# Optimization experiments

Hardware: AMD Instinct MI355X
Metric: run time of the kernel (lower is better)

The kernel has to match this reference:

```python
import jax, jax.numpy as jnp
import numpy as np

E, H, FF = 1024, 16, 4096
HD = E // H
B, S = 4, 2048


def _ln(x, g, b, eps=1e-5):
    m = jnp.mean(x, axis=-1, keepdims=True)
    v = jnp.mean((x - m) ** 2, axis=-1, keepdims=True)
    return (x - m) / jnp.sqrt(v + eps) * g + b


def setup_inputs() -> dict:
    k = jax.random.key(0)
    ks = jax.random.split(k, 12)
    sd = 0.02
    return {
        "value": jax.random.normal(ks[0], (B, S, E), jnp.float32),
        "key": jax.random.normal(ks[1], (B, S, E), jnp.float32),
        "query": jax.random.normal(ks[2], (B, S, E), jnp.float32),
        "mask": jnp.ones((B, 1, 1, S), jnp.int32),
        "Wv": sd * jax.random.normal(ks[3], (E, E), jnp.float32),
        "Wk": sd * jax.random.normal(ks[4], (E, E), jnp.float32),
        "Wq": sd * jax.random.normal(ks[5], (E, E), jnp.float32),
        "Wo": sd * jax.random.normal(ks[6], (E, E), jnp.float32),
        "bo": jnp.zeros((E,), jnp.float32),
        "ln1_g": jnp.ones((E,), jnp.float32), "ln1_b": jnp.zeros((E,), jnp.float32),
        "ln2_g": jnp.ones((E,), jnp.float32), "ln2_b": jnp.zeros((E,), jnp.float32),
        "lnf_g": jnp.ones((E,), jnp.float32), "lnf_b": jnp.zeros((E,), jnp.float32),
        "W1": sd * jax.random.normal(ks[7], (E, FF), jnp.float32),
        "b1": jnp.zeros((FF,), jnp.float32),
        "W2": sd * jax.random.normal(ks[8], (FF, E), jnp.float32),
        "b2": jnp.zeros((E,), jnp.float32),
    }


def reference(value, key, query, mask, Wv, Wk, Wq, Wo, bo,
              ln1_g, ln1_b, ln2_g, ln2_b, lnf_g, lnf_b, W1, b1, W2, b2):
    N, Sq, Em = query.shape
    # pre-norms (value & key share prenorm2 params, as in the torch module)
    v = _ln(value, ln2_g, ln2_b)
    k = _ln(key, ln2_g, ln2_b)
    q = _ln(query, ln1_g, ln1_b)
    # QKV projections (no bias), split heads
    V = (v @ Wv).reshape(N, v.shape[1], H, HD)
    K = (k @ Wk).reshape(N, k.shape[1], H, HD)
    Q = (q @ Wq).reshape(N, Sq, H, HD)
    energy = jnp.einsum("nqhd,nkhd->nhqk", Q, K)  # [N,H,Sq,Sk]
    energy = jnp.where(mask == 0, jnp.float32(-1e20), energy)
    attn = jax.nn.softmax(energy / jnp.float32(HD ** 0.5), axis=-1)
    out = jnp.einsum("nhqk,nkhd->nqhd", attn, V).reshape(N, Sq, Em)
    out = out @ Wo + bo
    x = out + q  # residual (drop_path is identity in eval)
    f = _ln(x, lnf_g, lnf_b) @ W1 + b1
    f = jax.nn.gelu(f, approximate=False) @ W2 + b2
    return f + x
```

## Files before the change

### kernel.cpp

```cpp
#include <hip/hip_runtime.h>
#include <hip/hip_bf16.h>
#include <math.h>

typedef __bf16 bf16x8 __attribute__((ext_vector_type(8)));
typedef __bf16 bf16x4 __attribute__((ext_vector_type(4)));
typedef float f32x4 __attribute__((ext_vector_type(4)));

#define AS1 __attribute__((address_space(1)))
#define AS3 __attribute__((address_space(3)))

__device__ __forceinline__ void gll16(const __bf16* g, __bf16* l) {
    __builtin_amdgcn_global_load_lds((const AS1 unsigned int*)g,
                                     (AS3 unsigned int*)l, 16, 0, 0);
}

__global__ __launch_bounds__(256) void transpose_w(const float* __restrict__ W,
                                                   __bf16* __restrict__ Wt,
                                                   int K, int N) {
    __shared__ float tile[32][33];
    int n0 = blockIdx.x * 32, k0 = blockIdx.y * 32;
    int tx = threadIdx.x & 31, ty = threadIdx.x >> 5;
    #pragma unroll
    for (int j = ty; j < 32; j += 8)
        tile[j][tx] = W[(size_t)(k0 + j) * N + n0 + tx];
    __syncthreads();
    #pragma unroll
    for (int j = ty; j < 32; j += 8)
        Wt[(size_t)(n0 + j) * K + k0 + tx] = (__bf16)tile[tx][j];
}

__global__ __launch_bounds__(256) void ln_kernel(const float* __restrict__ x,
                                                 const float* __restrict__ g,
                                                 const float* __restrict__ bb,
                                                 float* __restrict__ out32,
                                                 __bf16* __restrict__ outbf) {
    const int E = 1024;
    size_t row = blockIdx.x;
    int t = threadIdx.x;
    const float4* xr = (const float4*)(x + row * E);
    float4 v = xr[t];
    float s  = v.x + v.y + v.z + v.w;
    float s2 = v.x * v.x + v.y * v.y + v.z * v.z + v.w * v.w;
    #pragma unroll
    for (int off = 32; off >= 1; off >>= 1) {
        s  += __shfl_down(s, off);
        s2 += __shfl_down(s2, off);
    }
    __shared__ float red[2][4];
    int wid = t >> 6, lane = t & 63;
    if (lane == 0) { red[0][wid] = s; red[1][wid] = s2; }
    __syncthreads();
    if (t == 0) {
        float S1 = red[0][0] + red[0][1] + red[0][2] + red[0][3];
        float S2 = red[1][0] + red[1][1] + red[1][2] + red[1][3];
        float mean = S1 / E;
        float var  = S2 / E - mean * mean;
        red[0][0] = mean;
        red[1][0] = 1.0f / sqrtf(var + 1e-5f);
    }
    __syncthreads();
    float mean = red[0][0], rstd = red[1][0];
    float4 gv = ((const float4*)g)[t];
    float4 bv = ((const float4*)bb)[t];
    float y0 = (v.x - mean) * rstd * gv.x + bv.x;
    float y1 = (v.y - mean) * rstd * gv.y + bv.y;
    float y2 = (v.z - mean) * rstd * gv.z + bv.z;
    float y3 = (v.w - mean) * rstd * gv.w + bv.w;
    if (out32) ((float4*)(out32 + row * E))[t] = make_float4(y0, y1, y2, y3);
    if (outbf) {
        bf16x4 o;
        o[0] = (__bf16)y0; o[1] = (__bf16)y1; o[2] = (__bf16)y2; o[3] = (__bf16)y3;
        ((bf16x4*)(outbf + row * E))[t] = o;
    }
}

template <int EPI>
__global__ __launch_bounds__(256) void gemm128(const __bf16* __restrict__ A,
                                               const __bf16* __restrict__ Bt,
                                               const float* __restrict__ bias,
                                               const float* __restrict__ resid,
                                               void* __restrict__ Cout,
                                               int M, int N, int K) {
    __shared__ __bf16 As[128 * 64];
    __shared__ __bf16 Bs[128 * 64];
    int tid  = threadIdx.x;
    int lane = tid & 63, wid = tid >> 6;
    int quad = lane >> 4, l15 = lane & 15;
    int waveM = wid >> 1, waveN = wid & 1;
    size_t rowBase = (size_t)blockIdx.y * 128;
    size_t colBase = (size_t)blockIdx.x * 128;

    int lrow8  = lane >> 3;
    int lchunk = (lane & 7) ^ lrow8;
    const __bf16* Ag0 = A  + (rowBase + wid * 32 + lrow8) * (size_t)K + lchunk * 8;
    const __bf16* Bg0 = Bt + (colBase + wid * 32 + lrow8) * (size_t)K + lchunk * 8;
    __bf16* AsB = &As[(wid * 32) * 64];
    __bf16* BsB = &Bs[(wid * 32) * 64];

    f32x4 acc[4][4] = {};
    int swz = l15 & 7;

    for (int kb = 0; kb < K; kb += 64) {
        __syncthreads();
        #pragma unroll
        for (int i = 0; i < 4; i++) {
            gll16(Ag0 + (size_t)i * 8 * K + kb, AsB + i * 512);
            gll16(Bg0 + (size_t)i * 8 * K + kb, BsB + i * 512);
        }
        __syncthreads();
        #pragma unroll
        for (int ks = 0; ks < 2; ks++) {
            int p = ((ks * 4 + quad) ^ swz) * 8;
            bf16x8 af[4], bfr[4];
            #pragma unroll
            for (int mi = 0; mi < 4; mi++) {
                int m = waveM * 64 + mi * 16 + l15;
                af[mi] = *(const bf16x8*)&As[m * 64 + p];
            }
            #pragma unroll
            for (int ni = 0; ni < 4; ni++) {
                int n = waveN * 64 + ni * 16 + l15;
                bfr[ni] = *(const bf16x8*)&Bs[n * 64 + p];
            }
            #pragma unroll
            for (int mi = 0; mi < 4; mi++)
                #pragma unroll
                for (int ni = 0; ni < 4; ni++)
                    acc[mi][ni] = __builtin_amdgcn_mfma_f32_16x16x32_bf16(
                        af[mi], bfr[ni], acc[mi][ni], 0, 0, 0);
        }
    }

    #pragma unroll
    for (int mi = 0; mi < 4; mi++)
    #pragma unroll
    for (int ni = 0; ni < 4; ni++) {
        size_t col = colBase + waveN * 64 + ni * 16 + l15;
        if (EPI == 3) {
            size_t m0 = rowBase + waveM * 64 + mi * 16 + quad * 4;
            bf16x4 pk;
            #pragma unroll
            for (int r = 0; r < 4; r++) pk[r] = (__bf16)acc[mi][ni][r];
            *(bf16x4*)((__bf16*)Cout + col * M + m0) = pk;
        } else {
            #pragma unroll
            for (int r = 0; r < 4; r++) {
                size_t row = rowBase + waveM * 64 + mi * 16 + quad * 4 + r;
                float v = acc[mi][ni][r];
                if (EPI == 1) {
                    ((float*)Cout)[row * N + col] = v + bias[col] + resid[row * N + col];
                } else if (EPI == 2) {
                    float t2 = v + bias[col];
                    float gl = 0.5f * t2 * (1.0f + erff(t2 * 0.70710678118654752f));
                    ((__bf16*)Cout)[row * N + col] = (__bf16)gl;
                } else {
                    ((__bf16*)Cout)[row * N + col] = (__bf16)v;
                }
            }
        }
    }
}

__global__ __launch_bounds__(256) void attn_kernel(const __bf16* __restrict__ Q,
                                                   const __bf16* __restrict__ Kg,
                                                   const __bf16* __restrict__ Vt,
                                                   const int* __restrict__ mask,
                                                   __bf16* __restrict__ Out) {
    const int S = 2048, E = 1024, M = 8192;
    int qt = blockIdx.x, bh = blockIdx.y;
    int b = bh >> 4, h = bh & 15;
    int q0 = qt * 128;
    int tid = threadIdx.x, lane = tid & 63, wid = tid >> 6;
    int quad = lane >> 4, l15 = lane & 15;

    __shared__ __bf16 Ks[64][72];
    __shared__ __bf16 Vs[64][72];
    __shared__ __bf16 Ps[128][68];

    bf16x8 aq[2][2];
    #pragma unroll
    for (int m = 0; m < 2; m++)
        #pragma unroll
        for (int ks = 0; ks < 2; ks++) {
            size_t row = (size_t)(b * S + q0 + wid * 32 + m * 16 + l15);
            aq[m][ks] = *(const bf16x8*)(Q + row * E + h * 64 + ks * 32 + quad * 8);
        }

    int srow = tid >> 2;
    int scol = (tid & 3) * 16;
    const __bf16* Kbase = Kg + (size_t)(b * S) * E + h * 64;
    const __bf16* Vbase = Vt + (size_t)(h * 64 + srow) * M + b * S;

    bf16x8 kp0, kp1, vp0, vp1;
    kp0 = *(const bf16x8*)(Kbase + (size_t)srow * E + scol);
    kp1 = *(const bf16x8*)(Kbase + (size_t)srow * E + scol + 8);
    vp0 = *(const bf16x8*)(Vbase + scol);
    vp1 = *(const bf16x8*)(Vbase + scol + 8);

    f32x4 accO[2][4] = {};
    float accl[2][4] = {};

    for (int kt = 0; kt < S / 64; kt++) {
        int k0 = kt * 64;
        __syncthreads();
        *(bf16x8*)&Ks[srow][scol]     = kp0;
        *(bf16x8*)&Ks[srow][scol + 8] = kp1;
        *(bf16x8*)&Vs[srow][scol]     = vp0;
        *(bf16x8*)&Vs[srow][scol + 8] = vp1;
        __syncthreads();
        if (kt + 1 < S / 64) {
            int kn = k0 + 64;
            kp0 = *(const bf16x8*)(Kbase + (size_t)(kn + srow) * E + scol);
            kp1 = *(const bf16x8*)(Kbase + (size_t)(kn + srow) * E + scol + 8);
            vp0 = *(const bf16x8*)(Vbase + kn + scol);
            vp1 = *(const bf16x8*)(Vbase + kn + scol + 8);
        }

        f32x4 sa[2][4];
        #pragma unroll
        for (int nt = 0; nt < 4; nt++) {
            bf16x8 b0 = *(const bf16x8*)&Ks[nt * 16 + l15][quad * 8];
            bf16x8 b1 = *(const bf16x8*)&Ks[nt * 16 + l15][32 + quad * 8];
            #pragma unroll
            for (int m = 0; m < 2; m++) {
                f32x4 a = {};
                a = __builtin_amdgcn_mfma_f32_16x16x32_bf16(aq[m][0], b0, a, 0, 0, 0);
                a = __builtin_amdgcn_mfma_f32_16x16x32_bf16(aq[m][1], b1, a, 0, 0, 0);
                sa[m][nt] = a;
            }
        }

        #pragma unroll
        for (int nt = 0; nt < 4; nt++) {
            bool mz = (mask[b * S + k0 + nt * 16 + l15] == 0);
            #pragma unroll
            for (int m = 0; m < 2; m++)
                #pragma unroll
                for (int r = 0; r < 4; r++) {
                    float p = mz ? 0.0f : __expf(sa[m][nt][r] * 0.125f);
                    accl[m][r] += p;
                    Ps[wid * 32 + m * 16 + quad * 4 + r][nt * 16 + l15] = (__bf16)p;
                }
        }

        bf16x8 ap[2][2];
        #pragma unroll
        for (int m = 0; m < 2; m++)
            #pragma unroll
            for (int ks = 0; ks < 2; ks++)
                ap[m][ks] = *(const bf16x8*)&Ps[wid * 32 + m * 16 + l15][ks * 32 + quad * 8];

        #pragma unroll
        for (int nt = 0; nt < 4; nt++) {
            bf16x8 bv0 = *(const bf16x8*)&Vs[nt * 16 + l15][quad * 8];
            bf16x8 bv1 = *(const bf16x8*)&Vs[nt * 16 + l15][32 + quad * 8];
            #pragma unroll
            for (int m = 0; m < 2; m++) {
                accO[m][nt] = __builtin_amdgcn_mfma_f32_16x16x32_bf16(ap[m][0], bv0, accO[m][nt], 0, 0, 0);
                accO[m][nt] = __builtin_amdgcn_mfma_f32_16x16x32_bf16(ap[m][1], bv1, accO[m][nt], 0, 0, 0);
            }
        }
    }

    #pragma unroll
    for (int m = 0; m < 2; m++)
        #pragma unroll
        for (int r = 0; r < 4; r++) {
            float l = accl[m][r];
            #pragma unroll
            for (int off = 1; off < 16; off <<= 1) l += __shfl_xor(l, off);
            accl[m][r] = 1.0f / l;
        }

    #pragma unroll
    for (int m = 0; m < 2; m++)
        #pragma unroll
        for (int nt = 0; nt < 4; nt++)
            #pragma unroll
            for (int r = 0; r < 4; r++) {
                size_t row = (size_t)(b * S + q0 + wid * 32 + m * 16 + quad * 4 + r);
                Out[row * E + h * 64 + nt * 16 + l15] =
                    (__bf16)(accO[m][nt][r] * accl[m][r]);
            }
}

extern "C" void kernel_launch(void* const* d_in, const int* in_sizes, int n_in,
                              void* d_out, int out_size, void* d_ws, size_t ws_size,
                              hipStream_t stream) {
    const int Bb = 4, S = 2048, E = 1024, FF = 4096;
    const int M = Bb * S;

    const float* value = (const float*)d_in[0];
    const float* key   = (const float*)d_in[1];
    const float* query = (const float*)d_in[2];
    const int*   mask  = (const int*)d_in[3];
    const float* Wv    = (const float*)d_in[4];
    const float* Wk    = (const float*)d_in[5];
    const float* Wq    = (const float*)d_in[6];
    const float* Wo    = (const float*)d_in[7];
    const float* bo    = (const float*)d_in[8];
    const float* ln1_g = (const float*)d_in[9];
    const float* ln1_b = (const float*)d_in[10];
    const float* ln2_g = (const float*)d_in[11];
    const float* ln2_b = (const float*)d_in[12];
    const float* lnf_g = (const float*)d_in[13];
    const float* lnf_b = (const float*)d_in[14];
    const float* W1    = (const float*)d_in[15];
    const float* b1    = (const float*)d_in[16];
    const float* W2    = (const float*)d_in[17];
    const float* b2    = (const float*)d_in[18];

    char* ws = (char*)d_ws;
    const size_t MB = 1024 * 1024;
    __bf16* Wqt = (__bf16*)(ws + 0 * MB);
    __bf16* Wkt = (__bf16*)(ws + 2 * MB);
    __bf16* Wvt = (__bf16*)(ws + 4 * MB);
    __bf16* Wot = (__bf16*)(ws + 6 * MB);
    __bf16* W1t = (__bf16*)(ws + 8 * MB);
    __bf16* W2t = (__bf16*)(ws + 16 * MB);
    __bf16* q_bf = (__bf16*)(ws + 24 * MB);
    __bf16* k_bf = (__bf16*)(ws + 40 * MB);
    __bf16* v_bf = (__bf16*)(ws + 56 * MB);
    __bf16* Qb   = (__bf16*)(ws + 72 * MB);
    __bf16* Kb   = (__bf16*)(ws + 88 * MB);
    __bf16* Vtg  = (__bf16*)(ws + 104 * MB);
    __bf16* attn = q_bf;
    __bf16* x_ln = k_bf;
    __bf16* h1   = v_bf;
    float*  qln  = (float*)(ws + 120 * MB);
    float*  x32  = (float*)(ws + 152 * MB);

    transpose_w<<<dim3(E / 32, E / 32), 256, 0, stream>>>(Wq, Wqt, E, E);
    transpose_w<<<dim3(E / 32, E / 32), 256, 0, stream>>>(Wk, Wkt, E, E);
    transpose_w<<<dim3(E / 32, E / 32), 256, 0, stream>>>(Wv, Wvt, E, E);
    transpose_w<<<dim3(E / 32, E / 32), 256, 0, stream>>>(Wo, Wot, E, E);
    transpose_w<<<dim3(FF / 32, E / 32), 256, 0, stream>>>(W1, W1t, E, FF);
    transpose_w<<<dim3(E / 32, FF / 32), 256, 0, stream>>>(W2, W2t, FF, E);

    ln_kernel<<<M, 256, 0, stream>>>(query, ln1_g, ln1_b, qln, q_bf);
    ln_kernel<<<M, 256, 0, stream>>>(key, ln2_g, ln2_b, nullptr, k_bf);
    ln_kernel<<<M, 256, 0, stream>>>(value, ln2_g, ln2_b, nullptr, v_bf);

    gemm128<0><<<dim3(E / 128, M / 128), 256, 0, stream>>>(q_bf, Wqt, nullptr, nullptr, Qb, M, E, E);
    gemm128<0><<<dim3(E / 128, M / 128), 256, 0, stream>>>(k_bf, Wkt, nullptr, nullptr, Kb, M, E, E);
    gemm128<3><<<dim3(E / 128, M / 128), 256, 0, stream>>>(v_bf, Wvt, nullptr, nullptr, Vtg, M, E, E);

    attn_kernel<<<dim3(S / 128, Bb * 16), 256, 0, stream>>>(Qb, Kb, Vtg, mask, attn);

    gemm128<1><<<dim3(E / 128, M / 128), 256, 0, stream>>>(attn, Wot, bo, qln, x32, M, E, E);

    ln_kernel<<<M, 256, 0, stream>>>(x32, lnf_g, lnf_b, nullptr, x_ln);

    gemm128<2><<<dim3(FF / 128, M / 128), 256, 0, stream>>>(x_ln, W1t, b1, nullptr, h1, M, FF, E);
    gemm128<1><<<dim3(E / 128, M / 128), 256, 0, stream>>>(h1, W2t, b2, x32, (float*)d_out, M, E, FF);
}
```

Measured before the change: 719.8 us.

## Merge launches, fuse Q/K GEMMs, and rework attention with register-resident P

```diff
diff --git a/kernel.cpp b/kernel.cpp
--- a/kernel.cpp
+++ b/kernel.cpp
@@ -14,11 +14,35 @@
                                      (AS3 unsigned int*)l, 16, 0, 0);
 }
 
-__global__ __launch_bounds__(256) void transpose_w(const float* __restrict__ W,
-                                                   __bf16* __restrict__ Wt,
-                                                   int K, int N) {
+__device__ __forceinline__ unsigned pkbf(float a, float b) {
+    union { __bf16 h[2]; unsigned u; } t;
+    t.h[0] = (__bf16)a; t.h[1] = (__bf16)b;
+    return t.u;
+}
+
+__global__ __launch_bounds__(256) void transpose_all(
+    const float* __restrict__ Wq, const float* __restrict__ Wk,
+    const float* __restrict__ Wv, const float* __restrict__ Wo,
+    const float* __restrict__ W1, const float* __restrict__ W2,
+    __bf16* __restrict__ Wqt, __bf16* __restrict__ Wkt,
+    __bf16* __restrict__ Wvt, __bf16* __restrict__ Wot,
+    __bf16* __restrict__ W1t, __bf16* __restrict__ W2t) {
+    int g = blockIdx.x;
+    const float* W; __bf16* Wt; int K, N, kt, nt;
+    if (g < 4096) {
+        int mi = g >> 10, loc = g & 1023;
+        K = 1024; N = 1024; kt = loc >> 5; nt = loc & 31;
+        W  = mi == 0 ? Wq  : mi == 1 ? Wk  : mi == 2 ? Wv  : Wo;
+        Wt = mi == 0 ? Wqt : mi == 1 ? Wkt : mi == 2 ? Wvt : Wot;
+    } else if (g < 8192) {
+        int loc = g - 4096; W = W1; Wt = W1t;
+        K = 1024; N = 4096; kt = loc >> 7; nt = loc & 127;
+    } else {
+        int loc = g - 8192; W = W2; Wt = W2t;
+        K = 4096; N = 1024; kt = loc >> 5; nt = loc & 31;
+    }
+    int k0 = kt * 32, n0 = nt * 32;
     __shared__ float tile[32][33];
-    int n0 = blockIdx.x * 32, k0 = blockIdx.y * 32;
     int tx = threadIdx.x & 31, ty = threadIdx.x >> 5;
     #pragma unroll
     for (int j = ty; j < 32; j += 8)
@@ -29,18 +53,26 @@
         Wt[(size_t)(n0 + j) * K + k0 + tx] = (__bf16)tile[tx][j];
 }
 
-__global__ __launch_bounds__(256) void ln_kernel(const float* __restrict__ x,
-                                                 const float* __restrict__ g,
-                                                 const float* __restrict__ bb,
-                                                 float* __restrict__ out32,
-                                                 __bf16* __restrict__ outbf) {
+__global__ __launch_bounds__(256) void ln3_kernel(
+    const float* __restrict__ q, const float* __restrict__ k,
+    const float* __restrict__ v,
+    const float* __restrict__ g1, const float* __restrict__ b1,
+    const float* __restrict__ g2, const float* __restrict__ b2,
+    float* __restrict__ qln, __bf16* __restrict__ qbf,
+    __bf16* __restrict__ kbf, __bf16* __restrict__ vbf) {
     const int E = 1024;
+    int which = blockIdx.y;
+    const float* x = which == 0 ? q : which == 1 ? k : v;
+    const float* g = which == 0 ? g1 : g2;
+    const float* bb = which == 0 ? b1 : b2;
+    float* o32 = which == 0 ? qln : nullptr;
+    __bf16* obf = which == 0 ? qbf : which == 1 ? kbf : vbf;
+
     size_t row = blockIdx.x;
     int t = threadIdx.x;
-    const float4* xr = (const float4*)(x + row * E);
-    float4 v = xr[t];
-    float s  = v.x + v.y + v.z + v.w;
-    float s2 = v.x * v.x + v.y * v.y + v.z * v.z + v.w * v.w;
+    float4 val = ((const float4*)(x + row * E))[t];
+    float s  = val.x + val.y + val.z + val.w;
+    float s2 = val.x * val.x + val.y * val.y + val.z * val.z + val.w * val.w;
     #pragma unroll
     for (int off = 32; off >= 1; off >>= 1) {
         s  += __shfl_down(s, off);
@@ -62,25 +94,65 @@
     float mean = red[0][0], rstd = red[1][0];
     float4 gv = ((const float4*)g)[t];
     float4 bv = ((const float4*)bb)[t];
-    float y0 = (v.x - mean) * rstd * gv.x + bv.x;
-    float y1 = (v.y - mean) * rstd * gv.y + bv.y;
-    float y2 = (v.z - mean) * rstd * gv.z + bv.z;
-    float y3 = (v.w - mean) * rstd * gv.w + bv.w;
-    if (out32) ((float4*)(out32 + row * E))[t] = make_float4(y0, y1, y2, y3);
-    if (outbf) {
-        bf16x4 o;
-        o[0] = (__bf16)y0; o[1] = (__bf16)y1; o[2] = (__bf16)y2; o[3] = (__bf16)y3;
-        ((bf16x4*)(outbf + row * E))[t] = o;
-    }
+    float y0 = (val.x - mean) * rstd * gv.x + bv.x;
+    float y1 = (val.y - mean) * rstd * gv.y + bv.y;
+    float y2 = (val.z - mean) * rstd * gv.z + bv.z;
+    float y3 = (val.w - mean) * rstd * gv.w + bv.w;
+    if (o32) ((float4*)(o32 + row * E))[t] = make_float4(y0, y1, y2, y3);
+    bf16x4 o;
+    o[0] = (__bf16)y0; o[1] = (__bf16)y1; o[2] = (__bf16)y2; o[3] = (__bf16)y3;
+    ((bf16x4*)(obf + row * E))[t] = o;
+}
+
+__global__ __launch_bounds__(256) void ln_kernel(const float* __restrict__ x,
+                                                 const float* __restrict__ g,
+                                                 const float* __restrict__ bb,
+                                                 __bf16* __restrict__ outbf) {
+    const int E = 1024;
+    size_t row = blockIdx.x;
+    int t = threadIdx.x;
+    float4 v = ((const float4*)(x + row * E))[t];
+    float s  = v.x + v.y + v.z + v.w;
+    float s2 = v.x * v.x + v.y * v.y + v.z * v.z + v.w * v.w;
+    #pragma unroll
+    for (int off = 32; off >= 1; off >>= 1) {
+        s  += __shfl_down(s, off);
+        s2 += __shfl_down(s2, off);
+    }
+    __shared__ float red[2][4];
+    int wid = t >> 6, lane = t & 63;
+    if (lane == 0) { red[0][wid] = s; red[1][wid] = s2; }
+    __syncthreads();
+    if (t == 0) {
+        float S1 = red[0][0] + red[0][1] + red[0][2] + red[0][3];
+        float S2 = red[1][0] + red[1][1] + red[1][2] + red[1][3];
+        float mean = S1 / E;
+        float var  = S2 / E - mean * mean;
+        red[0][0] = mean;
+        red[1][0] = 1.0f / sqrtf(var + 1e-5f);
+    }
+    __syncthreads();
+    float mean = red[0][0], rstd = red[1][0];
+    float4 gv = ((const float4*)g)[t];
+    float4 bv = ((const float4*)bb)[t];
+    bf16x4 o;
+    o[0] = (__bf16)((v.x - mean) * rstd * gv.x + bv.x);
+    o[1] = (__bf16)((v.y - mean) * rstd * gv.y + bv.y);
+    o[2] = (__bf16)((v.z - mean) * rstd * gv.z + bv.z);
+    o[3] = (__bf16)((v.w - mean) * rstd * gv.w + bv.w);
+    ((bf16x4*)(outbf + row * E))[t] = o;
 }
 
 template <int EPI>
 __global__ __launch_bounds__(256) void gemm128(const __bf16* __restrict__ A,
+                                               const __bf16* __restrict__ A2,
                                                const __bf16* __restrict__ Bt,
+                                               const __bf16* __restrict__ Bt2,
                                                const float* __restrict__ bias,
                                                const float* __restrict__ resid,
                                                void* __restrict__ Cout,
-                                               int M, int N, int K) {
+                                               int M, int N, int K,
+                                               int splitN, float scale) {
     __shared__ __bf16 As[128 * 64];
     __shared__ __bf16 Bs[128 * 64];
     int tid  = threadIdx.x;
@@ -90,6 +162,93 @@
     size_t rowBase = (size_t)blockIdx.y * 128;
     size_t colBase = (size_t)blockIdx.x * 128;
 
+    const __bf16* Ap = A; const __bf16* Bp = Bt;
+    size_t colLoc = colBase;
+    float sc = scale;
+    if ((int)colBase >= splitN) { Ap = A2; Bp = Bt2; colLoc = colBase - splitN; sc = 1.0f; }
+
+    int lrow8  = lane >> 3;
+    int lchunk = (lane & 7) ^ lrow8;
+    const __bf16* Ag0 = Ap + (rowBase + wid * 32 + lrow8) * (size_t)K + lchunk * 8;
+    const __bf16* Bg0 = Bp + (colLoc  + wid * 32 + lrow8) * (size_t)K + lchunk * 8;
+    __bf16* AsB = &As[(wid * 32) * 64];
+    __bf16* BsB = &Bs[(wid * 32) * 64];
+
+    f32x4 acc[4][4] = {};
+    int swz = l15 & 7;
+
+    for (int kb = 0; kb < K; kb += 64) {
+        __syncthreads();
+        #pragma unroll
+        for (int i = 0; i < 4; i++) {
+            gll16(Ag0 + (size_t)i * 8 * K + kb, AsB + i * 512);
+            gll16(Bg0 + (size_t)i * 8 * K + kb, BsB + i * 512);
+        }
+        __syncthreads();
+        #pragma unroll
+        for (int ks = 0; ks < 2; ks++) {
+            int p = ((ks * 4 + quad) ^ swz) * 8;
+            bf16x8 af[4], bfr[4];
+            #pragma unroll
+            for (int mi = 0; mi < 4; mi++)
+                af[mi] = *(const bf16x8*)&As[(waveM * 64 + mi * 16 + l15) * 64 + p];
+            #pragma unroll
+            for (int ni = 0; ni < 4; ni++)
+                bfr[ni] = *(const bf16x8*)&Bs[(waveN * 64 + ni * 16 + l15) * 64 + p];
+            #pragma unroll
+            for (int mi = 0; mi < 4; mi++)
+                #pragma unroll
+                for (int ni = 0; ni < 4; ni++)
+                    acc[mi][ni] = __builtin_amdgcn_mfma_f32_16x16x32_bf16(
+                        bfr[ni], af[mi], acc[mi][ni], 0, 0, 0);
+        }
+    }
+
+    #pragma unroll
+    for (int mi = 0; mi < 4; mi++)
+    #pragma unroll
+    for (int ni = 0; ni < 4; ni++) {
+        size_t row = rowBase + waveM * 64 + mi * 16 + l15;
+        size_t col = colBase + waveN * 64 + ni * 16 + quad * 4;
+        f32x4 v = acc[mi][ni];
+        if (EPI == 1) {
+            float4 b4 = *(const float4*)&bias[col];
+            float4 r4 = *(const float4*)&resid[row * N + col];
+            float4 o;
+            o.x = v[0] + b4.x + r4.x; o.y = v[1] + b4.y + r4.y;
+            o.z = v[2] + b4.z + r4.z; o.w = v[3] + b4.w + r4.w;
+            *(float4*)&((float*)Cout)[row * N + col] = o;
+        } else if (EPI == 2) {
+            float4 b4 = *(const float4*)&bias[col];
+            bf16x4 pk;
+            #pragma unroll
+            for (int r = 0; r < 4; r++) {
+                float t2 = v[r] + ((const float*)&b4)[r];
+                pk[r] = (__bf16)(0.5f * t2 * (1.0f + erff(t2 * 0.70710678118654752f)));
+            }
+            *(bf16x4*)&((__bf16*)Cout)[row * N + col] = pk;
+        } else {
+            bf16x4 pk;
+            #pragma unroll
+            for (int r = 0; r < 4; r++) pk[r] = (__bf16)(v[r] * sc);
+            *(bf16x4*)&((__bf16*)Cout)[row * N + col] = pk;
+        }
+    }
+}
+
+__global__ __launch_bounds__(256) void gemmV(const __bf16* __restrict__ A,
+                                             const __bf16* __restrict__ Bt,
+                                             __bf16* __restrict__ Cout,
+                                             int M, int N, int K) {
+    __shared__ __bf16 As[128 * 64];
+    __shared__ __bf16 Bs[128 * 64];
+    int tid  = threadIdx.x;
+    int lane = tid & 63, wid = tid >> 6;
+    int quad = lane >> 4, l15 = lane & 15;
+    int waveM = wid >> 1, waveN = wid & 1;
+    size_t rowBase = (size_t)blockIdx.y * 128;
+    size_t colBase = (size_t)blockIdx.x * 128;
+
     int lrow8  = lane >> 3;
     int lchunk = (lane & 7) ^ lrow8;
     const __bf16* Ag0 = A  + (rowBase + wid * 32 + lrow8) * (size_t)K + lchunk * 8;
@@ -113,15 +272,11 @@
             int p = ((ks * 4 + quad) ^ swz) * 8;
             bf16x8 af[4], bfr[4];
             #pragma unroll
-            for (int mi = 0; mi < 4; mi++) {
-                int m = waveM * 64 + mi * 16 + l15;
-                af[mi] = *(const bf16x8*)&As[m * 64 + p];
-            }
-            #pragma unroll
-            for (int ni = 0; ni < 4; ni++) {
-                int n = waveN * 64 + ni * 16 + l15;
-                bfr[ni] = *(const bf16x8*)&Bs[n * 64 + p];
-            }
+            for (int mi = 0; mi < 4; mi++)
+                af[mi] = *(const bf16x8*)&As[(waveM * 64 + mi * 16 + l15) * 64 + p];
+            #pragma unroll
+            for (int ni = 0; ni < 4; ni++)
+                bfr[ni] = *(const bf16x8*)&Bs[(waveN * 64 + ni * 16 + l15) * 64 + p];
             #pragma unroll
             for (int mi = 0; mi < 4; mi++)
                 #pragma unroll
@@ -136,152 +291,160 @@
     #pragma unroll
     for (int ni = 0; ni < 4; ni++) {
         size_t col = colBase + waveN * 64 + ni * 16 + l15;
-        if (EPI == 3) {
-            size_t m0 = rowBase + waveM * 64 + mi * 16 + quad * 4;
-            bf16x4 pk;
-            #pragma unroll
-            for (int r = 0; r < 4; r++) pk[r] = (__bf16)acc[mi][ni][r];
-            *(bf16x4*)((__bf16*)Cout + col * M + m0) = pk;
-        } else {
-            #pragma unroll
-            for (int r = 0; r < 4; r++) {
-                size_t row = rowBase + waveM * 64 + mi * 16 + quad * 4 + r;
-                float v = acc[mi][ni][r];
-                if (EPI == 1) {
-                    ((float*)Cout)[row * N + col] = v + bias[col] + resid[row * N + col];
-                } else if (EPI == 2) {
-                    float t2 = v + bias[col];
-                    float gl = 0.5f * t2 * (1.0f + erff(t2 * 0.70710678118654752f));
-                    ((__bf16*)Cout)[row * N + col] = (__bf16)gl;
-                } else {
-                    ((__bf16*)Cout)[row * N + col] = (__bf16)v;
-                }
-            }
-        }
-    }
-}
-
-__global__ __launch_bounds__(256) void attn_kernel(const __bf16* __restrict__ Q,
-                                                   const __bf16* __restrict__ Kg,
+        size_t m0  = rowBase + waveM * 64 + mi * 16 + quad * 4;
+        bf16x4 pk;
+        #pragma unroll
+        for (int r = 0; r < 4; r++) pk[r] = (__bf16)acc[mi][ni][r];
+        *(bf16x4*)&Cout[col * M + m0] = pk;
+    }
+}
+
+__global__ __launch_bounds__(256) void attn_kernel(const __bf16* __restrict__ QK,
                                                    const __bf16* __restrict__ Vt,
                                                    const int* __restrict__ mask,
                                                    __bf16* __restrict__ Out) {
-    const int S = 2048, E = 1024, M = 8192;
+    const int S = 2048, E = 1024, E2 = 2048, M = 8192;
     int qt = blockIdx.x, bh = blockIdx.y;
     int b = bh >> 4, h = bh & 15;
     int q0 = qt * 128;
     int tid = threadIdx.x, lane = tid & 63, wid = tid >> 6;
     int quad = lane >> 4, l15 = lane & 15;
 
-    __shared__ __bf16 Ks[64][72];
-    __shared__ __bf16 Vs[64][72];
-    __shared__ __bf16 Ps[128][68];
+    __shared__ __bf16 KV[2][2 * 4096];
 
     bf16x8 aq[2][2];
     #pragma unroll
     for (int m = 0; m < 2; m++)
         #pragma unroll
-        for (int ks = 0; ks < 2; ks++) {
+        for (int hh = 0; hh < 2; hh++) {
             size_t row = (size_t)(b * S + q0 + wid * 32 + m * 16 + l15);
-            aq[m][ks] = *(const bf16x8*)(Q + row * E + h * 64 + ks * 32 + quad * 8);
-        }
-
-    int srow = tid >> 2;
-    int scol = (tid & 3) * 16;
-    const __bf16* Kbase = Kg + (size_t)(b * S) * E + h * 64;
-    const __bf16* Vbase = Vt + (size_t)(h * 64 + srow) * M + b * S;
-
-    bf16x8 kp0, kp1, vp0, vp1;
-    kp0 = *(const bf16x8*)(Kbase + (size_t)srow * E + scol);
-    kp1 = *(const bf16x8*)(Kbase + (size_t)srow * E + scol + 8);
-    vp0 = *(const bf16x8*)(Vbase + scol);
-    vp1 = *(const bf16x8*)(Vbase + scol + 8);
+            aq[m][hh] = *(const bf16x8*)(QK + row * E2 + h * 64 + hh * 32 + quad * 8);
+        }
+
+    int lrow8  = lane >> 3;
+    int lchunk = (lane & 7) ^ lrow8;
+    const __bf16* Kg0 = QK + (size_t)(b * S + wid * 16 + lrow8) * E2 + 1024 + h * 64 + lchunk * 8;
+    const __bf16* Vg0 = Vt + (size_t)(h * 64 + wid * 16 + lrow8) * M + b * S + lchunk * 8;
+
+    int srcA = ((quad & 1) * 2) * 16 + l15;
+    int srcB = srcA + 16;
+    bool selHi = (quad >= 2);
+    int swz = l15 & 7;
 
     f32x4 accO[2][4] = {};
-    float accl[2][4] = {};
+    float accl[2] = {0.f, 0.f};
+
+    {
+        __bf16* Kd = &KV[0][(wid * 16) * 64];
+        __bf16* Vd = &KV[0][4096 + (wid * 16) * 64];
+        #pragma unroll
+        for (int i = 0; i < 2; i++) {
+            gll16(Kg0 + (size_t)i * 8 * E2, Kd + i * 512);
+            gll16(Vg0 + (size_t)i * 8 * M,  Vd + i * 512);
+        }
+    }
+    __syncthreads();
 
     for (int kt = 0; kt < S / 64; kt++) {
         int k0 = kt * 64;
-        __syncthreads();
-        *(bf16x8*)&Ks[srow][scol]     = kp0;
-        *(bf16x8*)&Ks[srow][scol + 8] = kp1;
-        *(bf16x8*)&Vs[srow][scol]     = vp0;
-        *(bf16x8*)&Vs[srow][scol + 8] = vp1;
-        __syncthreads();
+        int buf = kt & 1;
         if (kt + 1 < S / 64) {
             int kn = k0 + 64;
-            kp0 = *(const bf16x8*)(Kbase + (size_t)(kn + srow) * E + scol);
-            kp1 = *(const bf16x8*)(Kbase + (size_t)(kn + srow) * E + scol + 8);
-            vp0 = *(const bf16x8*)(Vbase + kn + scol);
-            vp1 = *(const bf16x8*)(Vbase + kn + scol + 8);
-        }
+            __bf16* Kd = &KV[buf ^ 1][(wid * 16) * 64];
+            __bf16* Vd = &KV[buf ^ 1][4096 + (wid * 16) * 64];
+            #pragma unroll
+            for (int i = 0; i < 2; i++) {
+                gll16(Kg0 + (size_t)(kn + i * 8) * E2, Kd + i * 512);
+                gll16(Vg0 + (size_t)i * 8 * M + kn,    Vd + i * 512);
+            }
+        }
+        const __bf16* Ksb = &KV[buf][0];
+        const __bf16* Vsb = &KV[buf][4096];
 
         f32x4 sa[2][4];
         #pragma unroll
         for (int nt = 0; nt < 4; nt++) {
-            bf16x8 b0 = *(const bf16x8*)&Ks[nt * 16 + l15][quad * 8];
-            bf16x8 b1 = *(const bf16x8*)&Ks[nt * 16 + l15][32 + quad * 8];
+            bf16x8 a0 = *(const bf16x8*)&Ksb[(nt * 16 + l15) * 64 + ((0 * 4 + quad) ^ swz) * 8];
+            bf16x8 a1 = *(const bf16x8*)&Ksb[(nt * 16 + l15) * 64 + ((1 * 4 + quad) ^ swz) * 8];
             #pragma unroll
             for (int m = 0; m < 2; m++) {
                 f32x4 a = {};
-                a = __builtin_amdgcn_mfma_f32_16x16x32_bf16(aq[m][0], b0, a, 0, 0, 0);
-                a = __builtin_amdgcn_mfma_f32_16x16x32_bf16(aq[m][1], b1, a, 0, 0, 0);
+                a = __builtin_amdgcn_mfma_f32_16x16x32_bf16(a0, aq[m][0], a, 0, 0, 0);
+                a = __builtin_amdgcn_mfma_f32_16x16x32_bf16(a1, aq[m][1], a, 0, 0, 0);
                 sa[m][nt] = a;
             }
         }
 
+        unsigned pd[2][4][2];
         #pragma unroll
         for (int nt = 0; nt < 4; nt++) {
-            bool mz = (mask[b * S + k0 + nt * 16 + l15] == 0);
-            #pragma unroll
-            for (int m = 0; m < 2; m++)
-                #pragma unroll
-                for (int r = 0; r < 4; r++) {
-                    float p = mz ? 0.0f : __expf(sa[m][nt][r] * 0.125f);
-                    accl[m][r] += p;
-                    Ps[wid * 32 + m * 16 + quad * 4 + r][nt * 16 + l15] = (__bf16)p;
-                }
-        }
-
-        bf16x8 ap[2][2];
+            int4 mz = *(const int4*)&mask[b * S + k0 + nt * 16 + quad * 4];
+            #pragma unroll
+            for (int m = 0; m < 2; m++) {
+                float p0 = mz.x ? __expf(sa[m][nt][0]) : 0.f;
+                float p1 = mz.y ? __expf(sa[m][nt][1]) : 0.f;
+                float p2 = mz.z ? __expf(sa[m][nt][2]) : 0.f;
+                float p3 = mz.w ? __expf(sa[m][nt][3]) : 0.f;
+                accl[m] += (p0 + p1) + (p2 + p3);
+                pd[m][nt][0] = pkbf(p0, p1);
+                pd[m][nt][1] = pkbf(p2, p3);
+            }
+        }
+
+        bf16x8 bfrag[2][2];
         #pragma unroll
         for (int m = 0; m < 2; m++)
             #pragma unroll
-            for (int ks = 0; ks < 2; ks++)
-                ap[m][ks] = *(const bf16x8*)&Ps[wid * 32 + m * 16 + l15][ks * 32 + quad * 8];
-
-        #pragma unroll
-        for (int nt = 0; nt < 4; nt++) {
-            bf16x8 bv0 = *(const bf16x8*)&Vs[nt * 16 + l15][quad * 8];
-            bf16x8 bv1 = *(const bf16x8*)&Vs[nt * 16 + l15][32 + quad * 8];
+            for (int hh = 0; hh < 2; hh++) {
+                int ntLo = 2 * hh;
+                unsigned dA0 = __shfl((int)pd[m][ntLo][0], srcA, 64);
+                unsigned dB0 = __shfl((int)pd[m][ntLo + 1][0], srcA, 64);
+                unsigned dA1 = __shfl((int)pd[m][ntLo][1], srcA, 64);
+                unsigned dB1 = __shfl((int)pd[m][ntLo + 1][1], srcA, 64);
+                unsigned dA2 = __shfl((int)pd[m][ntLo][0], srcB, 64);
+                unsigned dB2 = __shfl((int)pd[m][ntLo + 1][0], srcB, 64);
+                unsigned dA3 = __shfl((int)pd[m][ntLo][1], srcB, 64);
+                unsigned dB3 = __shfl((int)pd[m][ntLo + 1][1], srcB, 64);
+                union { unsigned u[4]; bf16x8 v; } w;
+                w.u[0] = selHi ? dB0 : dA0;
+                w.u[1] = selHi ? dB1 : dA1;
+                w.u[2] = selHi ? dB2 : dA2;
+                w.u[3] = selHi ? dB3 : dA3;
+                bfrag[m][hh] = w.v;
+            }
+
+        #pragma unroll
+        for (int dt = 0; dt < 4; dt++) {
+            bf16x8 v0 = *(const bf16x8*)&Vsb[(dt * 16 + l15) * 64 + ((0 * 4 + quad) ^ swz) * 8];
+            bf16x8 v1 = *(const bf16x8*)&Vsb[(dt * 16 + l15) * 64 + ((1 * 4 + quad) ^ swz) * 8];
             #pragma unroll
             for (int m = 0; m < 2; m++) {
-                accO[m][nt] = __builtin_amdgcn_mfma_f32_16x16x32_bf16(ap[m][0], bv0, accO[m][nt], 0, 0, 0);
-                accO[m][nt] = __builtin_amdgcn_mfma_f32_16x16x32_bf16(ap[m][1], bv1, accO[m][nt], 0, 0, 0);
+                accO[m][dt] = __builtin_amdgcn_mfma_f32_16x16x32_bf16(v0, bfrag[m][0], accO[m][dt], 0, 0, 0);
+                accO[m][dt] = __builtin_amdgcn_mfma_f32_16x16x32_bf16(v1, bfrag[m][1], accO[m][dt], 0, 0, 0);
             }
         }
+        __syncthreads();
+    }
+
+    float inv[2];
+    #pragma unroll
+    for (int m = 0; m < 2; m++) {
+        float l = accl[m];
+        l += __shfl_xor(l, 16, 64);
+        l += __shfl_xor(l, 32, 64);
+        inv[m] = 1.0f / l;
     }
 
     #pragma unroll
     for (int m = 0; m < 2; m++)
         #pragma unroll
-        for (int r = 0; r < 4; r++) {
-            float l = accl[m][r];
-            #pragma unroll
-            for (int off = 1; off < 16; off <<= 1) l += __shfl_xor(l, off);
-            accl[m][r] = 1.0f / l;
-        }
-
-    #pragma unroll
-    for (int m = 0; m < 2; m++)
-        #pragma unroll
-        for (int nt = 0; nt < 4; nt++)
-            #pragma unroll
-            for (int r = 0; r < 4; r++) {
-                size_t row = (size_t)(b * S + q0 + wid * 32 + m * 16 + quad * 4 + r);
-                Out[row * E + h * 64 + nt * 16 + l15] =
-                    (__bf16)(accO[m][nt][r] * accl[m][r]);
-            }
+        for (int dt = 0; dt < 4; dt++) {
+            size_t row = (size_t)(b * S + q0 + wid * 32 + m * 16 + l15);
+            bf16x4 pk;
+            #pragma unroll
+            for (int r = 0; r < 4; r++) pk[r] = (__bf16)(accO[m][dt][r] * inv[m]);
+            *(bf16x4*)&Out[row * E + h * 64 + dt * 16 + quad * 4] = pk;
+        }
 }
 
 extern "C" void kernel_launch(void* const* d_in, const int* in_sizes, int n_in,
@@ -321,8 +484,7 @@
     __bf16* q_bf = (__bf16*)(ws + 24 * MB);
     __bf16* k_bf = (__bf16*)(ws + 40 * MB);
     __bf16* v_bf = (__bf16*)(ws + 56 * MB);
-    __bf16* Qb   = (__bf16*)(ws + 72 * MB);
-    __bf16* Kb   = (__bf16*)(ws + 88 * MB);
+    __bf16* QKb  = (__bf16*)(ws + 72 * MB);
     __bf16* Vtg  = (__bf16*)(ws + 104 * MB);
     __bf16* attn = q_bf;
     __bf16* x_ln = k_bf;
@@ -330,27 +492,27 @@
     float*  qln  = (float*)(ws + 120 * MB);
     float*  x32  = (float*)(ws + 152 * MB);
 
-    transpose_w<<<dim3(E / 32, E / 32), 256, 0, stream>>>(Wq, Wqt, E, E);
-    transpose_w<<<dim3(E / 32, E / 32), 256, 0, stream>>>(Wk, Wkt, E, E);
-    transpose_w<<<dim3(E / 32, E / 32), 256, 0, stream>>>(Wv, Wvt, E, E);
-    transpose_w<<<dim3(E / 32, E / 32), 256, 0, stream>>>(Wo, Wot, E, E);
-    transpose_w<<<dim3(FF / 32, E / 32), 256, 0, stream>>>(W1, W1t, E, FF);
-    transpose_w<<<dim3(E / 32, FF / 32), 256, 0, stream>>>(W2, W2t, FF, E);
-
-    ln_kernel<<<M, 256, 0, stream>>>(query, ln1_g, ln1_b, qln, q_bf);
-    ln_kernel<<<M, 256, 0, stream>>>(key, ln2_g, ln2_b, nullptr, k_bf);
-    ln_kernel<<<M, 256, 0, stream>>>(value, ln2_g, ln2_b, nullptr, v_bf);
-
-    gemm128<0><<<dim3(E / 128, M / 128), 256, 0, stream>>>(q_bf, Wqt, nullptr, nullptr, Qb, M, E, E);
-    gemm128<0><<<dim3(E / 128, M / 128), 256, 0, stream>>>(k_bf, Wkt, nullptr, nullptr, Kb, M, E, E);
-    gemm128<3><<<dim3(E / 128, M / 128), 256, 0, stream>>>(v_bf, Wvt, nullptr, nullptr, Vtg, M, E, E);
-
-    attn_kernel<<<dim3(S / 128, Bb * 16), 256, 0, stream>>>(Qb, Kb, Vtg, mask, attn);
-
-    gemm128<1><<<dim3(E / 128, M / 128), 256, 0, stream>>>(attn, Wot, bo, qln, x32, M, E, E);
-
-    ln_kernel<<<M, 256, 0, stream>>>(x32, lnf_g, lnf_b, nullptr, x_ln);
-
-    gemm128<2><<<dim3(FF / 128, M / 128), 256, 0, stream>>>(x_ln, W1t, b1, nullptr, h1, M, FF, E);
-    gemm128<1><<<dim3(E / 128, M / 128), 256, 0, stream>>>(h1, W2t, b2, x32, (float*)d_out, M, E, FF);
-}
+    transpose_all<<<12288, 256, 0, stream>>>(Wq, Wk, Wv, Wo, W1, W2,
+                                             Wqt, Wkt, Wvt, Wot, W1t, W2t);
+
+    ln3_kernel<<<dim3(M, 3), 256, 0, stream>>>(query, key, value,
+                                               ln1_g, ln1_b, ln2_g, ln2_b,
+                                               qln, q_bf, k_bf, v_bf);
+
+    gemm128<0><<<dim3(2 * E / 128, M / 128), 256, 0, stream>>>(
+        q_bf, k_bf, Wqt, Wkt, nullptr, nullptr, QKb, M, 2 * E, E, E, 0.125f);
+
+    gemmV<<<dim3(E / 128, M / 128), 256, 0, stream>>>(v_bf, Wvt, Vtg, M, E, E);
+
+    attn_kernel<<<dim3(S / 128, Bb * 16), 256, 0, stream>>>(QKb, Vtg, mask, attn);
+
+    gemm128<1><<<dim3(E / 128, M / 128), 256, 0, stream>>>(
+        attn, attn, Wot, Wot, bo, qln, x32, M, E, E, E, 1.0f);
+
+    ln_kernel<<<M, 256, 0, stream>>>(x32, lnf_g, lnf_b, x_ln);
+
+    gemm128<2><<<dim3(FF / 128, M / 128), 256, 0, stream>>>(
+        x_ln, x_ln, W1t, W1t, b1, nullptr, h1, M, FF, E, FF, 1.0f);
+    gemm128<1><<<dim3(E / 128, M / 128), 256, 0, stream>>>(
+        h1, h1, W2t, W2t, b2, x32, (float*)d_out, M, E, FF, E, 1.0f);
+}
```

Result: no change. 721.1 us (+0.2%).
